# Kernel optimization log

Measured on AMD Instinct MI355X. Metric: run time of the kernel, lower is better.

Reference implementation:

```python
import jax, jax.numpy as jnp
import numpy as np

TAU_B = 0.1
MARGIN_OV = 0.3
MARGIN_DIV = 0.8

B, D = 131072, 256
C, K = 8, 2


def _normalize(x, axis=-1):
    n = jnp.linalg.norm(x, axis=axis, keepdims=True)
    return x / jnp.maximum(n, 1e-12)


def setup_inputs() -> dict:
    key = jax.random.key(0)
    k1, k2, k3, k4, k5 = jax.random.split(key, 5)
    z = jax.random.normal(k1, (B, D), dtype=jnp.float32)
    labels = jax.random.randint(k2, (B,), 0, C, dtype=jnp.int64)
    sample_rel = jax.random.uniform(k3, (B, 1), dtype=jnp.float32)
    ball_centers = jax.random.normal(k4, (C, K, D), dtype=jnp.float32)
    ball_radii = jnp.full((C, K), 0.2, dtype=jnp.float32)
    return {"z": z, "labels": labels, "sample_rel": sample_rel,
            "ball_centers": ball_centers, "ball_radii": ball_radii}


def reference(z, labels, sample_rel, ball_centers, ball_radii):
    # Eval-mode forward (dropout inactive, no EMA buffer update).
    z_norm = _normalize(z)                       # [B, D]
    c_norm = _normalize(ball_centers)            # [C, K, D]
    radii = jnp.clip(jnp.abs(ball_radii), 0.05, 1.0)  # [C, K]

    # --- intra loss: vectorized replacement of the per-sample python loop ---
    c_k = c_norm[labels]                         # gather [B, K, D]
    sim = jnp.einsum('bd,bkd->bk', z_norm, c_k)  # [B, K]
    dist = 1.0 - sim
    q = jax.lax.stop_gradient(jax.nn.softmax(sim / TAU_B, axis=-1))  # detached
    dist_w = jnp.sum(q * dist, axis=-1)          # [B]
    r_w = jnp.sum(q * radii[labels], axis=-1)    # [B]
    L_intra = jnp.mean(sample_rel[:, 0] * jax.nn.relu(dist_w - r_w))

    # --- overlap loss over all centers, block-diagonal (same-class) masked ---
    c_flat = c_norm.reshape(C * K, D)
    sim_matrix = c_flat @ c_flat.T               # [CK, CK]
    ids = jnp.repeat(jnp.arange(C), K)
    mask = (ids[:, None] != ids[None, :]).astype(sim_matrix.dtype)
    L_overlap = jnp.sum(jax.nn.relu(sim_matrix - MARGIN_OV) * mask) / (jnp.sum(mask) + 1e-6)

    # --- diversity loss: within-class pairs p < q ---
    sim_within = jnp.einsum('cpd,cqd->cpq', c_norm, c_norm)  # [C, K, K]
    triu = jnp.triu(jnp.ones((K, K), dtype=sim_within.dtype), k=1)
    div_count = C * K * (K - 1) // 2
    L_div = jnp.sum(jax.nn.relu(sim_within - MARGIN_DIV) * triu) / div_count

    L_total = 1.0 * L_intra + 0.5 * L_overlap + 0.5 * L_div
    return L_total
```

## Files before the change

### kernel.cpp

```cpp
#include <hip/hip_runtime.h>
#include <math.h>

#define B_N    131072
#define D_DIM  256
#define D4     64
#define NC     16
#define NBLK   2048
#define TAU_INV    10.0f
#define MARGIN_OV  0.3f
#define MARGIN_DIV 0.8f

__global__ __launch_bounds__(256) void fused_kernel(
    const float* __restrict__ z,
    const int*   __restrict__ labels,
    const float* __restrict__ rel,
    const float* __restrict__ centers,
    const float* __restrict__ radii,
    float* __restrict__ ws)
{
    __shared__ float sC[NC * D_DIM];
    __shared__ float sRed[12];

    const int tid = threadIdx.x;

    {
        const int ci = tid >> 4;
        const int gl = tid & 15;
        const float4* cr4 = (const float4*)centers;
        float4* sC4 = (float4*)sC;
        float4 cv[4];
        float ssq = 0.f;
        #pragma unroll
        for (int p = 0; p < 4; ++p) {
            cv[p] = cr4[ci * D4 + p * 16 + gl];
            ssq += cv[p].x*cv[p].x + cv[p].y*cv[p].y + cv[p].z*cv[p].z + cv[p].w*cv[p].w;
        }
        #pragma unroll
        for (int m = 1; m < 16; m <<= 1) ssq += __shfl_xor(ssq, m, 64);
        const float cinv = 1.0f / fmaxf(sqrtf(ssq), 1e-12f);
        #pragma unroll
        for (int p = 0; p < 4; ++p) {
            float4 v = cv[p];
            v.x *= cinv; v.y *= cinv; v.z *= cinv; v.w *= cinv;
            sC4[ci * D4 + p * 16 + gl] = v;
        }
    }
    __syncthreads();

    const int wv = (blockIdx.x << 2) + (tid >> 6);
    const int l  = tid & 15;
    const int g  = (tid >> 4) & 3;
    const float4* z4  = (const float4*)z;
    const float4* sC4 = (const float4*)sC;

    float acc = 0.f;
    #pragma unroll
    for (int t = 0; t < 4; ++t) {
        const int s   = (wv << 4) + (t << 2) + g;
        const int lbl = labels[s];

        float zz = 0.f, d0 = 0.f, d1 = 0.f;
        #pragma unroll
        for (int p = 0; p < 4; ++p) {
            const float4 zv = z4[s * D4 + p * 16 + l];
            const float4 a  = sC4[(lbl * 2 + 0) * D4 + p * 16 + l];
            const float4 b  = sC4[(lbl * 2 + 1) * D4 + p * 16 + l];
            zz += zv.x*zv.x + zv.y*zv.y + zv.z*zv.z + zv.w*zv.w;
            d0 += zv.x*a.x  + zv.y*a.y  + zv.z*a.z  + zv.w*a.w;
            d1 += zv.x*b.x  + zv.y*b.y  + zv.z*b.z  + zv.w*b.w;
        }
        #pragma unroll
        for (int m = 1; m < 16; m <<= 1) {
            zz += __shfl_xor(zz, m, 64);
            d0 += __shfl_xor(d0, m, 64);
            d1 += __shfl_xor(d1, m, 64);
        }
        const float invn = 1.0f / fmaxf(sqrtf(zz), 1e-12f);
        const float s0 = d0 * invn;
        const float s1 = d1 * invn;
        const float r0 = fminf(fmaxf(fabsf(radii[lbl * 2 + 0]), 0.05f), 1.0f);
        const float r1 = fminf(fmaxf(fabsf(radii[lbl * 2 + 1]), 0.05f), 1.0f);
        const float q0 = 1.0f / (1.0f + __expf((s1 - s0) * TAU_INV));
        const float val = q0 * ((1.0f - s0) - r0) + (1.0f - q0) * ((1.0f - s1) - r1);
        acc += (l == 0) ? rel[s] * fmaxf(val, 0.f) : 0.f;
    }

    float ovs = 0.f, dvs = 0.f;
    if (blockIdx.x == 0) {
        const int i = tid >> 4, j = tid & 15;
        float dot = 0.f;
        #pragma unroll 4
        for (int d = 0; d < D4; ++d) {
            const float4 a = sC4[i * D4 + d];
            const float4 b = sC4[j * D4 + d];
            dot += a.x*b.x + a.y*b.y + a.z*b.z + a.w*b.w;
        }
        if ((i >> 1) != (j >> 1))      ovs = fmaxf(dot - MARGIN_OV, 0.f);
        else if (i < j)                dvs = fmaxf(dot - MARGIN_DIV, 0.f);
    }

    #pragma unroll
    for (int m = 1; m < 64; m <<= 1) {
        acc += __shfl_xor(acc, m, 64);
        ovs += __shfl_xor(ovs, m, 64);
        dvs += __shfl_xor(dvs, m, 64);
    }
    const int w = tid >> 6;
    if ((tid & 63) == 0) { sRed[w] = acc; sRed[4 + w] = ovs; sRed[8 + w] = dvs; }
    __syncthreads();
    if (tid == 0) {
        ws[blockIdx.x] = sRed[0] + sRed[1] + sRed[2] + sRed[3];
        if (blockIdx.x == 0) {
            ws[NBLK + 0] = sRed[4] + sRed[5] + sRed[6] + sRed[7];
            ws[NBLK + 1] = sRed[8] + sRed[9] + sRed[10] + sRed[11];
        }
    }
}

__global__ __launch_bounds__(256) void finalize_kernel(
    const float* __restrict__ ws, float* __restrict__ out)
{
    __shared__ float sRed[4];
    const int tid = threadIdx.x;
    float a = 0.f;
    #pragma unroll
    for (int k = 0; k < NBLK / 256; ++k) a += ws[tid + k * 256];
    #pragma unroll
    for (int m = 1; m < 64; m <<= 1) a += __shfl_xor(a, m, 64);
    if ((tid & 63) == 0) sRed[tid >> 6] = a;
    __syncthreads();
    if (tid == 0) {
        const float intra = (sRed[0] + sRed[1] + sRed[2] + sRed[3]) * (1.0f / (float)B_N);
        const float l_ov  = ws[NBLK + 0] / (224.0f + 1e-6f);
        const float l_dv  = ws[NBLK + 1] * (1.0f / 8.0f);
        out[0] = intra + 0.5f * l_ov + 0.5f * l_dv;
    }
}

extern "C" void kernel_launch(void* const* d_in, const int* in_sizes, int n_in,
                              void* d_out, int out_size, void* d_ws, size_t ws_size,
                              hipStream_t stream) {
    const float* z       = (const float*)d_in[0];
    const int*   labels  = (const int*)d_in[1];
    const float* rel     = (const float*)d_in[2];
    const float* centers = (const float*)d_in[3];
    const float* radii   = (const float*)d_in[4];
    float* out = (float*)d_out;
    float* wsf = (float*)d_ws;

    fused_kernel<<<NBLK, 256, 0, stream>>>(z, labels, rel, centers, radii, wsf);
    finalize_kernel<<<1, 256, 0, stream>>>(wsf, out);
}
```

Measured before the change: 198.4 us.

## Prefetch z rows into registers before centers sync and pad shared centers

Changes the lane mapping to 8 lanes per sample with 2 samples per lane group, and issues all z, label, rel and radii loads at kernel start, before the center normalization and __syncthreads, so global loads overlap the prologue. It also pads the shared center rows to 65 float4s to reduce LDS bank conflicts on the label-dependent gathers. The cost is higher register use (16 float4 of z per thread), which may reduce occupancy.

```diff
diff --git a/kernel.cpp b/kernel.cpp
--- a/kernel.cpp
+++ b/kernel.cpp
@@ -5,6 +5,7 @@
 #define D_DIM  256
 #define D4     64
 #define NC     16
+#define CPAD   65
 #define NBLK   2048
 #define TAU_INV    10.0f
 #define MARGIN_OV  0.3f
@@ -18,10 +19,24 @@
     const float* __restrict__ radii,
     float* __restrict__ ws)
 {
-    __shared__ float sC[NC * D_DIM];
+    __shared__ float sC[NC * CPAD * 4];
     __shared__ float sRed[12];
 
     const int tid = threadIdx.x;
+    const int wv  = (blockIdx.x << 2) + (tid >> 6);
+    const int g   = (tid >> 3) & 7;
+    const int l   = tid & 7;
+
+    const int sA = (wv << 4) + g;
+    const int sB = sA + 8;
+    const int lblA = labels[sA];
+    const int lblB = labels[sB];
+    const float relA = rel[sA];
+    const float relB = rel[sB];
+    const float rA0 = fminf(fmaxf(fabsf(radii[lblA * 2 + 0]), 0.05f), 1.0f);
+    const float rA1 = fminf(fmaxf(fabsf(radii[lblA * 2 + 1]), 0.05f), 1.0f);
+    const float rB0 = fminf(fmaxf(fabsf(radii[lblB * 2 + 0]), 0.05f), 1.0f);
+    const float rB1 = fminf(fmaxf(fabsf(radii[lblB * 2 + 1]), 0.05f), 1.0f);
 
     {
         const int ci = tid >> 4;
@@ -42,35 +57,35 @@
         for (int p = 0; p < 4; ++p) {
             float4 v = cv[p];
             v.x *= cinv; v.y *= cinv; v.z *= cinv; v.w *= cinv;
-            sC4[ci * D4 + p * 16 + gl] = v;
+            sC4[ci * CPAD + p * 16 + gl] = v;
         }
     }
+
+    const float4* z4 = (const float4*)z;
+    float4 zA[8], zB[8];
+    #pragma unroll
+    for (int p = 0; p < 8; ++p) zA[p] = z4[sA * D4 + p * 8 + l];
+    #pragma unroll
+    for (int p = 0; p < 8; ++p) zB[p] = z4[sB * D4 + p * 8 + l];
+
     __syncthreads();
 
-    const int wv = (blockIdx.x << 2) + (tid >> 6);
-    const int l  = tid & 15;
-    const int g  = (tid >> 4) & 3;
-    const float4* z4  = (const float4*)z;
     const float4* sC4 = (const float4*)sC;
+    float acc = 0.f;
 
-    float acc = 0.f;
-    #pragma unroll
-    for (int t = 0; t < 4; ++t) {
-        const int s   = (wv << 4) + (t << 2) + g;
-        const int lbl = labels[s];
-
+    {
         float zz = 0.f, d0 = 0.f, d1 = 0.f;
         #pragma unroll
-        for (int p = 0; p < 4; ++p) {
-            const float4 zv = z4[s * D4 + p * 16 + l];
-            const float4 a  = sC4[(lbl * 2 + 0) * D4 + p * 16 + l];
-            const float4 b  = sC4[(lbl * 2 + 1) * D4 + p * 16 + l];
+        for (int p = 0; p < 8; ++p) {
+            const float4 zv = zA[p];
+            const float4 a  = sC4[(lblA * 2 + 0) * CPAD + p * 8 + l];
+            const float4 b  = sC4[(lblA * 2 + 1) * CPAD + p * 8 + l];
             zz += zv.x*zv.x + zv.y*zv.y + zv.z*zv.z + zv.w*zv.w;
             d0 += zv.x*a.x  + zv.y*a.y  + zv.z*a.z  + zv.w*a.w;
             d1 += zv.x*b.x  + zv.y*b.y  + zv.z*b.z  + zv.w*b.w;
         }
         #pragma unroll
-        for (int m = 1; m < 16; m <<= 1) {
+        for (int m = 1; m < 8; m <<= 1) {
             zz += __shfl_xor(zz, m, 64);
             d0 += __shfl_xor(d0, m, 64);
             d1 += __shfl_xor(d1, m, 64);
@@ -78,11 +93,34 @@
         const float invn = 1.0f / fmaxf(sqrtf(zz), 1e-12f);
         const float s0 = d0 * invn;
         const float s1 = d1 * invn;
-        const float r0 = fminf(fmaxf(fabsf(radii[lbl * 2 + 0]), 0.05f), 1.0f);
-        const float r1 = fminf(fmaxf(fabsf(radii[lbl * 2 + 1]), 0.05f), 1.0f);
         const float q0 = 1.0f / (1.0f + __expf((s1 - s0) * TAU_INV));
-        const float val = q0 * ((1.0f - s0) - r0) + (1.0f - q0) * ((1.0f - s1) - r1);
-        acc += (l == 0) ? rel[s] * fmaxf(val, 0.f) : 0.f;
+        const float val = q0 * ((1.0f - s0) - rA0) + (1.0f - q0) * ((1.0f - s1) - rA1);
+        acc += (l == 0) ? relA * fmaxf(val, 0.f) : 0.f;
+    }
+
+    {
+        float zz = 0.f, d0 = 0.f, d1 = 0.f;
+        #pragma unroll
+        for (int p = 0; p < 8; ++p) {
+            const float4 zv = zB[p];
+            const float4 a  = sC4[(lblB * 2 + 0) * CPAD + p * 8 + l];
+            const float4 b  = sC4[(lblB * 2 + 1) * CPAD + p * 8 + l];
+            zz += zv.x*zv.x + zv.y*zv.y + zv.z*zv.z + zv.w*zv.w;
+            d0 += zv.x*a.x  + zv.y*a.y  + zv.z*a.z  + zv.w*a.w;
+            d1 += zv.x*b.x  + zv.y*b.y  + zv.z*b.z  + zv.w*b.w;
+        }
+        #pragma unroll
+        for (int m = 1; m < 8; m <<= 1) {
+            zz += __shfl_xor(zz, m, 64);
+            d0 += __shfl_xor(d0, m, 64);
+            d1 += __shfl_xor(d1, m, 64);
+        }
+        const float invn = 1.0f / fmaxf(sqrtf(zz), 1e-12f);
+        const float s0 = d0 * invn;
+        const float s1 = d1 * invn;
+        const float q0 = 1.0f / (1.0f + __expf((s1 - s0) * TAU_INV));
+        const float val = q0 * ((1.0f - s0) - rB0) + (1.0f - q0) * ((1.0f - s1) - rB1);
+        acc += (l == 0) ? relB * fmaxf(val, 0.f) : 0.f;
     }
 
     float ovs = 0.f, dvs = 0.f;
@@ -91,8 +129,8 @@
         float dot = 0.f;
         #pragma unroll 4
         for (int d = 0; d < D4; ++d) {
-            const float4 a = sC4[i * D4 + d];
-            const float4 b = sC4[j * D4 + d];
+            const float4 a = sC4[i * CPAD + d];
+            const float4 b = sC4[j * CPAD + d];
             dot += a.x*b.x + a.y*b.y + a.z*b.z + a.w*b.w;
         }
         if ((i >> 1) != (j >> 1))      ovs = fmaxf(dot - MARGIN_OV, 0.f);
```

After: 198.1 us. Within noise of the previous version (-0.1%).

## Double-buffer z loads, halve block count, pad center smem, precompute radii

Applied to the files above, without the earlier changes.

Each block now handles twice as many samples, with 8 lanes per sample and 8 samples per wave per step. The next sample's z row, label and rel are prefetched into registers while the current one is computed, and the first prefetch is issued before the center-normalization barrier. Centers in shared memory get a padded row stride to avoid bank conflicts, and clamped radii are cached in shared memory. The goal is to hide global-load latency and cut launch and reduction overhead, at the cost of more registers (two buffers of 8 float4 each), which may lower occupancy.

```diff
diff --git a/kernel.cpp b/kernel.cpp
--- a/kernel.cpp
+++ b/kernel.cpp
@@ -5,7 +5,8 @@
 #define D_DIM  256
 #define D4     64
 #define NC     16
-#define NBLK   2048
+#define CPAD   65
+#define NBLK   1024
 #define TAU_INV    10.0f
 #define MARGIN_OV  0.3f
 #define MARGIN_DIV 0.8f
@@ -18,16 +19,23 @@
     const float* __restrict__ radii,
     float* __restrict__ ws)
 {
-    __shared__ float sC[NC * D_DIM];
+    __shared__ float sC[NC * CPAD * 4];
+    __shared__ float sRad[NC];
     __shared__ float sRed[12];
 
-    const int tid = threadIdx.x;
+    const int tid  = threadIdx.x;
+    const int wv   = (blockIdx.x << 2) + (tid >> 6);
+    const int g    = (tid >> 3) & 7;
+    const int l    = tid & 7;
+    const int base = (wv << 5) + g;
+
+    const float4* z4 = (const float4*)z;
 
     {
         const int ci = tid >> 4;
         const int gl = tid & 15;
         const float4* cr4 = (const float4*)centers;
-        float4* sC4 = (float4*)sC;
+        float4* sC4w = (float4*)sC;
         float4 cv[4];
         float ssq = 0.f;
         #pragma unroll
@@ -42,35 +50,56 @@
         for (int p = 0; p < 4; ++p) {
             float4 v = cv[p];
             v.x *= cinv; v.y *= cinv; v.z *= cinv; v.w *= cinv;
-            sC4[ci * D4 + p * 16 + gl] = v;
+            sC4w[ci * CPAD + p * 16 + gl] = v;
         }
+        if (tid < NC) sRad[tid] = fminf(fmaxf(fabsf(radii[tid]), 0.05f), 1.0f);
     }
+
+    float4 zb[2][8];
+    int   lblN;
+    float relN;
+    {
+        const int s = base;
+        #pragma unroll
+        for (int p = 0; p < 8; ++p) zb[0][p] = z4[s * D4 + p * 8 + l];
+        lblN = labels[s];
+        relN = rel[s];
+    }
+
     __syncthreads();
 
-    const int wv = (blockIdx.x << 2) + (tid >> 6);
-    const int l  = tid & 15;
-    const int g  = (tid >> 4) & 3;
-    const float4* z4  = (const float4*)z;
     const float4* sC4 = (const float4*)sC;
+    float acc = 0.f;
 
-    float acc = 0.f;
     #pragma unroll
-    for (int t = 0; t < 4; ++t) {
-        const int s   = (wv << 4) + (t << 2) + g;
-        const int lbl = labels[s];
+    for (int i = 0; i < 4; ++i) {
+        const int cur = i & 1, nxt = cur ^ 1;
+        const int   lbl  = lblN;
+        const float relC = relN;
+
+        if (i < 3) {
+            const int s = base + ((i + 1) << 3);
+            #pragma unroll
+            for (int p = 0; p < 8; ++p) zb[nxt][p] = z4[s * D4 + p * 8 + l];
+            lblN = labels[s];
+            relN = rel[s];
+        }
+
+        const float r0 = sRad[lbl * 2 + 0];
+        const float r1 = sRad[lbl * 2 + 1];
 
         float zz = 0.f, d0 = 0.f, d1 = 0.f;
         #pragma unroll
-        for (int p = 0; p < 4; ++p) {
-            const float4 zv = z4[s * D4 + p * 16 + l];
-            const float4 a  = sC4[(lbl * 2 + 0) * D4 + p * 16 + l];
-            const float4 b  = sC4[(lbl * 2 + 1) * D4 + p * 16 + l];
+        for (int p = 0; p < 8; ++p) {
+            const float4 zv = zb[cur][p];
+            const float4 a  = sC4[(lbl * 2 + 0) * CPAD + p * 8 + l];
+            const float4 b  = sC4[(lbl * 2 + 1) * CPAD + p * 8 + l];
             zz += zv.x*zv.x + zv.y*zv.y + zv.z*zv.z + zv.w*zv.w;
             d0 += zv.x*a.x  + zv.y*a.y  + zv.z*a.z  + zv.w*a.w;
             d1 += zv.x*b.x  + zv.y*b.y  + zv.z*b.z  + zv.w*b.w;
         }
         #pragma unroll
-        for (int m = 1; m < 16; m <<= 1) {
+        for (int m = 1; m < 8; m <<= 1) {
             zz += __shfl_xor(zz, m, 64);
             d0 += __shfl_xor(d0, m, 64);
             d1 += __shfl_xor(d1, m, 64);
@@ -78,11 +107,9 @@
         const float invn = 1.0f / fmaxf(sqrtf(zz), 1e-12f);
         const float s0 = d0 * invn;
         const float s1 = d1 * invn;
-        const float r0 = fminf(fmaxf(fabsf(radii[lbl * 2 + 0]), 0.05f), 1.0f);
-        const float r1 = fminf(fmaxf(fabsf(radii[lbl * 2 + 1]), 0.05f), 1.0f);
         const float q0 = 1.0f / (1.0f + __expf((s1 - s0) * TAU_INV));
         const float val = q0 * ((1.0f - s0) - r0) + (1.0f - q0) * ((1.0f - s1) - r1);
-        acc += (l == 0) ? rel[s] * fmaxf(val, 0.f) : 0.f;
+        acc += (l == 0) ? relC * fmaxf(val, 0.f) : 0.f;
     }
 
     float ovs = 0.f, dvs = 0.f;
@@ -91,8 +118,8 @@
         float dot = 0.f;
         #pragma unroll 4
         for (int d = 0; d < D4; ++d) {
-            const float4 a = sC4[i * D4 + d];
-            const float4 b = sC4[j * D4 + d];
+            const float4 a = sC4[i * CPAD + d];
+            const float4 b = sC4[j * CPAD + d];
             dot += a.x*b.x + a.y*b.y + a.z*b.z + a.w*b.w;
         }
         if ((i >> 1) != (j >> 1))      ovs = fmaxf(dot - MARGIN_OV, 0.f);
```

Measured after the change: 199.8 us. About the same (+0.7%).
